# Kernel tuning notes

Measured on AMD Instinct MI355X. Metric: run time of the kernel, lower is better.

## Reference

```python
import jax, jax.numpy as jnp
import numpy as np

B, T, D, H, L, V = 2, 1024, 1024, 16, 6, 32000
HD = D // H  # head_size = n_emb // n_heads
EPS = 1e-5   # torch LayerNorm default


def setup_inputs() -> dict:
    key = jax.random.key(0)
    ks = jax.random.split(key, 19)
    s = 0.02
    n = lambda k, shape: jax.random.normal(k, shape, dtype=jnp.float32) * s
    return {
        "idx": jax.random.randint(ks[0], (B, T), 0, V),
        "targets": jax.random.randint(ks[1], (B, T), 0, V),
        "tok_emb": n(ks[2], (V, D)),
        "pos_emb": n(ks[3], (V, D)),  # only first T rows used, as in the source
        "Wq": n(ks[4], (L, H, D, HD)),
        "Wk": n(ks[5], (L, H, D, HD)),
        "Wv": n(ks[6], (L, H, D, HD)),
        "Wo": n(ks[7], (L, D, D)),
        "bo": n(ks[8], (L, D)),
        "W1": n(ks[9], (L, D, 4 * D)),
        "b1": n(ks[10], (L, 4 * D)),
        "W2": n(ks[11], (L, 4 * D, D)),
        "b2": n(ks[12], (L, D)),
        "ln_g": jnp.ones((D,), jnp.float32),
        "ln_b": jnp.zeros((D,), jnp.float32),
        "Wf": n(ks[13], (D, V)),
        "bf": n(ks[14], (V,)),
    }


def _layer_norm(x, g, b):
    mu = jnp.mean(x, axis=-1, keepdims=True)
    var = jnp.mean(jnp.square(x - mu), axis=-1, keepdims=True)
    return (x - mu) * jax.lax.rsqrt(var + EPS) * g + b


def _forward(idx, targets, tok_emb, pos_emb, Wq, Wk, Wv, Wo, bo,
             W1, b1, W2, b2, ln_g, ln_b, Wf, bf):
    x = tok_emb[idx] + pos_emb[:T]  # [B,T,D]
    tril = jnp.tril(jnp.ones((T, T), dtype=bool))
    scale = jnp.asarray(D, x.dtype) ** -0.5  # NOTE: source scales by C=N_EMBED, not head_size

    def block(x, p):
        wq, wk, wv, wo, bo_, w1, b1_, w2, b2_ = p
        q = jnp.einsum('btd,hde->bhte', x, wq)
        k = jnp.einsum('btd,hde->bhte', x, wk)
        v = jnp.einsum('btd,hde->bhte', x, wv)
        scores = jnp.einsum('bhte,bhse->bhts', q, k) * scale
        scores = jnp.where(tril, scores, -jnp.inf)
        att = jax.nn.softmax(scores, axis=-1)
        o = jnp.einsum('bhts,bhse->bhte', att, v)
        o = o.transpose(0, 2, 1, 3).reshape(B, T, D)  # concat heads
        x = x + o @ wo + bo_                           # attn residual (no LN in source)
        h = jax.nn.relu(x @ w1 + b1_)
        x = x + h @ w2 + b2_                           # ffn residual
        return x, None

    x, _ = jax.lax.scan(block, x, (Wq, Wk, Wv, Wo, bo, W1, b1, W2, b2))
    x = _layer_norm(x, ln_g, ln_b)
    logits = x @ Wf + bf  # [B,T,V]
    logp = jax.nn.log_softmax(logits, axis=-1)
    nll = -jnp.take_along_axis(logp, targets[..., None], axis=-1)
    loss = jnp.mean(nll)
    return logits, loss


def reference(idx, targets, tok_emb, pos_emb, Wq, Wk, Wv, Wo, bo,
              W1, b1, W2, b2, ln_g, ln_b, Wf, bf):
    return _forward(idx, targets, tok_emb, pos_emb, Wq, Wk, Wv, Wo, bo,
                    W1, b1, W2, b2, ln_g, ln_b, Wf, bf)
```

## Files before the change

### kernel.cpp

```cpp
#include <hip/hip_runtime.h>
#include <hip/hip_bf16.h>

typedef unsigned short u16;
typedef unsigned int u32;
typedef float f32x4 __attribute__((ext_vector_type(4)));
typedef __bf16 bf16x8 __attribute__((ext_vector_type(8)));

#define NB 2
#define NT 1024
#define ND 1024
#define NH 16
#define HDIM 64
#define NL 6
#define NV 32000
#define ND4 4096
#define BT (NB * NT)
#define L2E 1.44269504f
#define NSLOT 500

__device__ __forceinline__ u16 f2b(float f) {
  u32 u = __builtin_bit_cast(u32, f);
  u32 r = (u + 0x7FFFu + ((u >> 16) & 1u)) >> 16;
  return (u16)r;
}

__device__ __forceinline__ void gl_lds16(const void* g, void* lds) {
  __builtin_amdgcn_global_load_lds((const __attribute__((address_space(1))) u32*)g,
                                   (__attribute__((address_space(3))) u32*)lds, 16, 0, 0);
}

__device__ __forceinline__ float rmax16(float v) {
  v = fmaxf(v, __shfl_xor(v, 1, 64));
  v = fmaxf(v, __shfl_xor(v, 2, 64));
  v = fmaxf(v, __shfl_xor(v, 4, 64));
  v = fmaxf(v, __shfl_xor(v, 8, 64));
  return v;
}
__device__ __forceinline__ float rsum16(float v) {
  v += __shfl_xor(v, 1, 64);
  v += __shfl_xor(v, 2, 64);
  v += __shfl_xor(v, 4, 64);
  v += __shfl_xor(v, 8, 64);
  return v;
}

__device__ __forceinline__ void tr512(const float* in, int in_rs, u16* out, int out_rs,
                                      int k0, int n0, float (*t)[65]) {
  int tid = threadIdx.x;
#pragma unroll
  for (int i = 0; i < 8; ++i) {
    int e = tid + 512 * i;
    int r = e >> 6, c = e & 63;
    t[r][c] = in[(size_t)(k0 + r) * in_rs + n0 + c];
  }
  __syncthreads();
#pragma unroll
  for (int i = 0; i < 8; ++i) {
    int e = tid + 512 * i;
    int r = e >> 6, c = e & 63;
    out[(size_t)(n0 + r) * out_rs + k0 + c] = f2b(t[c][r]);
  }
}

__device__ __forceinline__ void trans512_blk(
    int i, int l, const float* Wq, const float* Wk, const float* Wv,
    const float* Wo, const float* W1, const float* W2,
    u16* wqkvT, u16* woT, u16* w1T, u16* w2T, float (*t)[65]) {
  if (i < 768) {
    int x = i & 15, z = i >> 4;
    int s = z >> 4, h = z & 15;
    const float* in = (s == 0 ? Wq : s == 1 ? Wk : Wv) + ((size_t)(l * NH + h)) * ND * HDIM;
    u16* o = wqkvT + ((size_t)(s * ND + h * HDIM)) * ND;
    tr512(in, HDIM, o, ND, x * 64, 0, t);
  } else if (i < 1024) {
    int j = i - 768, x = j & 15, y = j >> 4;
    tr512(Wo + (size_t)l * ND * ND, ND, woT, ND, y * 64, x * 64, t);
  } else if (i < 2048) {
    int j = i - 1024, x = j & 63, y = j >> 6;
    tr512(W1 + (size_t)l * ND * ND4, ND4, w1T, ND, y * 64, x * 64, t);
  } else {
    int j = i - 2048, x = j & 15, y = j >> 4;
    tr512(W2 + (size_t)l * ND4 * ND, ND, w2T, ND4, y * 64, x * 64, t);
  }
}

__global__ void __launch_bounds__(512) k_pre(const int* __restrict__ idx,
                                             const float* __restrict__ tok,
                                             const float* __restrict__ pos,
                                             float* __restrict__ xf, u16* __restrict__ xb,
                                             const float* __restrict__ Wq,
                                             const float* __restrict__ Wk,
                                             const float* __restrict__ Wv,
                                             const float* __restrict__ Wo,
                                             const float* __restrict__ W1,
                                             const float* __restrict__ W2,
                                             u16* __restrict__ wT0) {
  __shared__ float t[64][65];
  int bid = blockIdx.x;
  if (bid < 1024) {
    int tid = threadIdx.x;
    int row = bid * 2 + (tid >> 8);
    int tt = row & (NT - 1);
    int tk = idx[row];
    int c = (tid & 255) * 4;
    float4 a = *(const float4*)(tok + (size_t)tk * ND + c);
    float4 p = *(const float4*)(pos + (size_t)tt * ND + c);
    float4 s = make_float4(a.x + p.x, a.y + p.y, a.z + p.z, a.w + p.w);
    *(float4*)(xf + (size_t)row * ND + c) = s;
    u16* o = xb + (size_t)row * ND + c;
    *(u32*)(o + 0) = (u32)f2b(s.x) | ((u32)f2b(s.y) << 16);
    *(u32*)(o + 2) = (u32)f2b(s.z) | ((u32)f2b(s.w) << 16);
    return;
  }
  trans512_blk(bid - 1024, 0, Wq, Wk, Wv, Wo, W1, W2,
               wT0, wT0 + (size_t)3 * ND * ND, wT0 + (size_t)4 * ND * ND,
               wT0 + (size_t)8 * ND * ND, t);
}

template <int EPI>
__global__ void __launch_bounds__(512, 2)
k_gemm8(const u16* __restrict__ A, const u16* __restrict__ Bt,
        const float* __restrict__ bias, float* __restrict__ outf,
        u16* __restrict__ outb, int K, int N, int nMt, float* __restrict__ pl) {
  __shared__ u16 lds[2][2][2][128 * 64];
  int tid = threadIdx.x;
  int w = tid >> 6, l = tid & 63;
  int l4 = l >> 4, lm = l & 15;
  int wm = w >> 2, wn = w & 3;

  int nwg = gridDim.x, bid = blockIdx.x;
  int q8 = nwg >> 3, r8 = nwg & 7;
  int xcd = bid & 7, loc = bid >> 3;
  int swz = (xcd < r8 ? xcd * (q8 + 1) : r8 * (q8 + 1) + (xcd - r8) * q8) + loc;
  int m0 = (swz % nMt) * 256;
  int n0 = (swz / nMt) * 256;

  f32x4 acc[8][4];
  f32x4 z = {0.f, 0.f, 0.f, 0.f};
#pragma unroll
  for (int m = 0; m < 8; ++m)
#pragma unroll
    for (int n = 0; n < 4; ++n) acc[m][n] = z;

  int srow = (w << 3) + (l >> 3);
  int scol = (((l & 7) ^ ((l >> 3) & 7)) << 3);
  int sdst = w * 512 + l * 8;

  auto stage_half = [&](int b, int mat, int h, int kt) {
    int k0 = kt << 6;
    const u16* base = (mat == 0 ? A + (size_t)(m0 + (h << 7)) * K
                                : Bt + (size_t)(n0 + (h << 7)) * K);
#pragma unroll
    for (int i = 0; i < 2; ++i)
      gl_lds16(base + (size_t)(i * 64 + srow) * K + k0 + scol,
               &lds[b][mat][h][i * 4096 + sdst]);
  };

  int c0 = (l4 ^ (lm & 7)) * 8;
  int c1 = c0 ^ 32;
  int brow0 = (wn & 1) * 64;

  const u16* A0h = &lds[0][0][wm][0];
  const u16* B0h = &lds[0][1][wn >> 1][0];
  const u16* A1h = &lds[1][0][wm][0];
  const u16* B1h = &lds[1][1][wn >> 1][0];

  bf16x8 Ar[4][2], Bx[2][2], By[2][2];

  auto dsA = [&](const u16* Ah, int mf0) {
#pragma unroll
    for (int mf = 0; mf < 4; ++mf) {
      Ar[mf][0] = *(const bf16x8*)&Ah[((mf0 + mf) * 16 + lm) * 64 + c0];
      Ar[mf][1] = *(const bf16x8*)&Ah[((mf0 + mf) * 16 + lm) * 64 + c1];
    }
  };
  auto dsB = [&](const u16* Bh, bf16x8 (&B)[2][2], int nf0) {
#pragma unroll
    for (int nf = 0; nf < 2; ++nf) {
      B[nf][0] = *(const bf16x8*)&Bh[(brow0 + (nf0 + nf) * 16 + lm) * 64 + c0];
      B[nf][1] = *(const bf16x8*)&Bh[(brow0 + (nf0 + nf) * 16 + lm) * 64 + c1];
    }
  };
  auto mm = [&](int am, bf16x8 (&B)[2][2], int an) {
    __builtin_amdgcn_s_setprio(1);
#pragma unroll
    for (int mf = 0; mf < 4; ++mf)
#pragma unroll
      for (int nf = 0; nf < 2; ++nf) {
        acc[am + mf][an + nf] =
            __builtin_amdgcn_mfma_f32_16x16x32_bf16(Ar[mf][0], B[nf][0], acc[am + mf][an + nf], 0, 0, 0);
        acc[am + mf][an + nf] =
            __builtin_amdgcn_mfma_f32_16x16x32_bf16(Ar[mf][1], B[nf][1], acc[am + mf][an + nf], 0, 0, 0);
      }
    __builtin_amdgcn_s_setprio(0);
  };
  auto openbar = [&]() {
    __builtin_amdgcn_sched_barrier(0);
    __builtin_amdgcn_s_barrier();
    __builtin_amdgcn_sched_barrier(0);
  };
  auto midbar = [&]() {
    __builtin_amdgcn_sched_barrier(0);
    __builtin_amdgcn_s_barrier();
    asm volatile("s_waitcnt lgkmcnt(0)" ::: "memory");
    __builtin_amdgcn_sched_barrier(0);
  };

  int nk = K >> 6;
  stage_half(0, 0, 0, 0); stage_half(0, 0, 1, 0);
  stage_half(0, 1, 0, 0); stage_half(0, 1, 1, 0);
  stage_half(1, 0, 0, 1);

  for (int u = 0; u < nk; u += 2) {
    bool s2 = (u + 2 < nk), s3 = (u + 3 < nk);
    asm volatile("s_waitcnt vmcnt(2)" ::: "memory");
    openbar();
    dsA(A0h, 0); dsB(B0h, Bx, 0);
    stage_half(1, 0, 1, u + 1);
    midbar();
    mm(0, Bx, 0);
    openbar();
    dsB(B0h, By, 2);
    stage_half(1, 1, 0, u + 1);
    midbar();
    mm(0, By, 2);
    openbar();
    dsA(A0h, 4);
    stage_half(1, 1, 1, u + 1);
    midbar();
    mm(4, By, 2);
    openbar();
    if (s2) stage_half(0, 0, 0, u + 2);
    midbar();
    mm(4, Bx, 0);
    if (s2) asm volatile("s_waitcnt vmcnt(2)" ::: "memory");
    else    asm volatile("s_waitcnt vmcnt(0)" ::: "memory");
    openbar();
    dsA(A1h, 0); dsB(B1h, Bx, 0);
    if (s2) stage_half(0, 0, 1, u + 2);
    midbar();
    mm(0, Bx, 0);
    openbar();
    dsB(B1h, By, 2);
    if (s2) stage_half(0, 1, 0, u + 2);
    midbar();
    mm(0, By, 2);
    openbar();
    dsA(A1h, 4);
    if (s2) stage_half(0, 1, 1, u + 2);
    midbar();
    mm(4, By, 2);
    openbar();
    if (s3) stage_half(1, 0, 0, u + 3);
    midbar();
    mm(4, Bx, 0);
  }

  if constexpr (EPI == 4) {
    int slot = (n0 >> 6) + wn;
#pragma unroll
    for (int mf = 0; mf < 8; ++mf)
#pragma unroll
      for (int j = 0; j < 4; ++j) {
        int row = m0 + wm * 128 + mf * 16 + l4 * 4 + j;
        float sm = 0.f;
#pragma unroll
        for (int nf = 0; nf < 4; ++nf) {
          int col = n0 + wn * 64 + nf * 16 + lm;
          float v = acc[mf][nf][j] + bias[col];
          __builtin_nontemporal_store(v, &outf[(size_t)row * N + col]);
          sm += exp2f(v * L2E);
        }
        sm = rsum16(sm);
        if (lm == 0) pl[(size_t)row * NSLOT + slot] = sm;
      }
  } else {
#pragma unroll
    for (int mf = 0; mf < 8; ++mf)
#pragma unroll
      for (int nf = 0; nf < 4; ++nf)
#pragma unroll
        for (int j = 0; j < 4; ++j) {
          int row = m0 + wm * 128 + mf * 16 + l4 * 4 + j;
          int col = n0 + wn * 64 + nf * 16 + lm;
          float v = acc[mf][nf][j];
          if constexpr (EPI == 0) outb[(size_t)row * N + col] = f2b(v);
          else __builtin_nontemporal_store(v + bias[col], &outf[(size_t)row * N + col]);
        }
  }
}

template <int EPI, int BN>
__global__ void __launch_bounds__(256, BN == 64 ? 3 : 2)
k_gemm4(const u16* __restrict__ A, const u16* __restrict__ Bt,
        const float* __restrict__ bias, float* __restrict__ outf,
        u16* __restrict__ outb, int K, int N, int nMt) {
  constexpr int NFW = BN / 32;
  constexpr int NH2 = NFW / 2;
  __shared__ u16 As[2][128 * 64];
  __shared__ u16 Bs[2][BN * 64];
  int tid = threadIdx.x;
  int w = tid >> 6, l = tid & 63;
  int l4 = l >> 4, lm = l & 15;
  int wr = w >> 1, wc = w & 1;

  int nwg = gridDim.x, bid = blockIdx.x;
  int q8 = nwg >> 3, r8 = nwg & 7;
  int xcd = bid & 7, loc = bid >> 3;
  int swz = (xcd < r8 ? xcd * (q8 + 1) : r8 * (q8 + 1) + (xcd - r8) * q8) + loc;
  int m0 = (swz % nMt) * 128;
  int n0 = (swz / nMt) * BN;

  f32x4 acc[4][NFW];
  f32x4 z = {0.f, 0.f, 0.f, 0.f};
#pragma unroll
  for (int m = 0; m < 4; ++m)
#pragma unroll
    for (int n = 0; n < NFW; ++n) acc[m][n] = z;

  int srow = (w << 3) + (l >> 3);
  int scol = (((l & 7) ^ ((l >> 3) & 7)) << 3);
  int sdst = w * 512 + l * 8;

  const u16* Arow = A + (size_t)m0 * K;
  const u16* Brow = Bt + (size_t)n0 * K;

  auto stage = [&](int b, int kt) {
    int k0 = kt << 6;
#pragma unroll
    for (int i = 0; i < 4; ++i)
      gl_lds16(Arow + (size_t)(i * 32 + srow) * K + k0 + scol, &As[b][i * 2048 + sdst]);
#pragma unroll
    for (int i = 0; i < BN / 32; ++i)
      gl_lds16(Brow + (size_t)(i * 32 + srow) * K + k0 + scol, &Bs[b][i * 2048 + sdst]);
  };

  int c0 = (l4 ^ (lm & 7)) * 8;
  int c1 = c0 ^ 32;

  int nk = K >> 6;
  stage(0, 0);
  for (int t = 0; t < nk; ++t) {
    int b = t & 1;
    asm volatile("s_waitcnt vmcnt(0)" ::: "memory");
    __builtin_amdgcn_sched_barrier(0);
    __builtin_amdgcn_s_barrier();
    __builtin_amdgcn_sched_barrier(0);
    if (t + 1 < nk) stage(b ^ 1, t + 1);
    __builtin_amdgcn_sched_barrier(0);

    bf16x8 af[4][2], bfr[NH2][2];
#pragma unroll
    for (int mf = 0; mf < 4; ++mf) {
      af[mf][0] = *(const bf16x8*)&As[b][(mf * 16 + lm) * 64 + c0 + (wr * 64 * 64)];
      af[mf][1] = *(const bf16x8*)&As[b][(mf * 16 + lm) * 64 + c1 + (wr * 64 * 64)];
    }
#pragma unroll
    for (int nf = 0; nf < NH2; ++nf) {
      int brow = wc * (BN / 2) + nf * 16 + lm;
      bfr[nf][0] = *(const bf16x8*)&Bs[b][brow * 64 + c0];
      bfr[nf][1] = *(const bf16x8*)&Bs[b][brow * 64 + c1];
    }
    __builtin_amdgcn_s_setprio(1);
#pragma unroll
    for (int mf = 0; mf < 4; ++mf)
#pragma unroll
      for (int nf = 0; nf < NH2; ++nf) {
        acc[mf][nf] = __builtin_amdgcn_mfma_f32_16x16x32_bf16(af[mf][0], bfr[nf][0], acc[mf][nf], 0, 0, 0);
        acc[mf][nf] = __builtin_amdgcn_mfma_f32_16x16x32_bf16(af[mf][1], bfr[nf][1], acc[mf][nf], 0, 0, 0);
      }
    __builtin_amdgcn_s_setprio(0);

#pragma unroll
    for (int nf = 0; nf < NH2; ++nf) {
      int brow = wc * (BN / 2) + (nf + NH2) * 16 + lm;
      bfr[nf][0] = *(const bf16x8*)&Bs[b][brow * 64 + c0];
      bfr[nf][1] = *(const bf16x8*)&Bs[b][brow * 64 + c1];
    }
    __builtin_amdgcn_s_setprio(1);
#pragma unroll
    for (int mf = 0; mf < 4; ++mf)
#pragma unroll
      for (int nf = 0; nf < NH2; ++nf) {
        acc[mf][nf + NH2] = __builtin_amdgcn_mfma_f32_16x16x32_bf16(af[mf][0], bfr[nf][0], acc[mf][nf + NH2], 0, 0, 0);
        acc[mf][nf + NH2] = __builtin_amdgcn_mfma_f32_16x16x32_bf16(af[mf][1], bfr[nf][1], acc[mf][nf + NH2], 0, 0, 0);
      }
    __builtin_amdgcn_s_setprio(0);
  }

#pragma unroll
  for (int mf = 0; mf < 4; ++mf)
#pragma unroll
    for (int nf = 0; nf < NFW; ++nf)
#pragma unroll
      for (int j = 0; j < 4; ++j) {
        int row = m0 + wr * 64 + mf * 16 + l4 * 4 + j;
        int col = n0 + wc * (BN / 2) + nf * 16 + lm;
        float v = acc[mf][nf][j];
        if constexpr (EPI == 0) {
          outb[(size_t)row * N + col] = f2b(v);
        } else if constexpr (EPI == 2) {
          v += bias[col];
          outb[(size_t)row * N + col] = f2b(fmaxf(v, 0.f));
        } else {
          v += bias[col];
          size_t o = (size_t)row * N + col;
          float nx = outf[o] + v;
          outf[o] = nx;
          outb[o] = f2b(nx);
        }
      }
}

__global__ void __launch_bounds__(512) k_attn_mega(
    const u16* __restrict__ qkv, u16* __restrict__ ob,
    const float* __restrict__ Wq, const float* __restrict__ Wk,
    const float* __restrict__ Wv, const float* __restrict__ Wo,
    const float* __restrict__ W1, const float* __restrict__ W2,
    const float* __restrict__ Wf, u16* __restrict__ wTnext,
    u16* __restrict__ wfT, int lNext) {
  __shared__ char smem[70656];
  int bid = blockIdx.x;
  if (bid >= 256) {
    auto t = reinterpret_cast<float(*)[65]>(smem);
    int i = bid - 256;
    if (lNext < NL) {
      trans512_blk(i, lNext, Wq, Wk, Wv, Wo, W1, W2,
                   wTnext, wTnext + (size_t)3 * ND * ND, wTnext + (size_t)4 * ND * ND,
                   wTnext + (size_t)8 * ND * ND, t);
    } else {
      int x = i % 500, y = i / 500;
      tr512(Wf, NV, wfT, ND, y * 64, x * 64, t);
    }
    return;
  }
  u16* Ks = (u16*)smem;
  u16* Vt = Ks + 128 * 72;
  u16* Pw = Vt + 64 * 136;
  int qb = bid & 7, h = (bid >> 3) & 15, b = bid >> 7;
  int tid = threadIdx.x;
  int w = tid >> 6, l = tid & 63;
  int l4 = l >> 4, lm = l & 15;

  const u16* base = qkv + (size_t)b * NT * 3072 + h * HDIM;

  bf16x8 qf[2];
#pragma unroll
  for (int kk = 0; kk < 2; ++kk) {
    int tq = qb * 128 + w * 16 + lm;
    qf[kk] = *(const bf16x8*)(base + (size_t)tq * 3072 + kk * 32 + l4 * 8);
  }

  int r0 = tid >> 3, e0 = (tid & 7) << 3;

  auto loadT = [&](int kb, bf16x8& k0, bf16x8& k1, bf16x8& v0, bf16x8& v1) {
    const u16* s0 = base + (size_t)(kb * 128 + r0) * 3072;
    const u16* s1 = s0 + (size_t)64 * 3072;
    k0 = *(const bf16x8*)(s0 + 1024 + e0);
    v0 = *(const bf16x8*)(s0 + 2048 + e0);
    k1 = *(const bf16x8*)(s1 + 1024 + e0);
    v1 = *(const bf16x8*)(s1 + 2048 + e0);
  };

  f32x4 z = {0.f, 0.f, 0.f, 0.f};
  f32x4 oacc[4];
  float mrow[4], lrow[4];
#pragma unroll
  for (int n = 0; n < 4; ++n) oacc[n] = z;
#pragma unroll
  for (int j = 0; j < 4; ++j) { mrow[j] = -1e30f; lrow[j] = 0.f; }

  bf16x8 ck0, ck1, cv0, cv1;
  loadT(0, ck0, ck1, cv0, cv1);
  bf16x8 nk0 = ck0, nk1 = ck1, nv0 = cv0, nv1 = cv1;

  for (int kb = 0; kb <= qb; ++kb) {
    __syncthreads();
    {
      *(bf16x8*)&Ks[r0 * 72 + e0] = ck0;
      *(bf16x8*)&Ks[(r0 + 64) * 72 + e0] = ck1;
      union { bf16x8 v; u16 u[8]; } a, c;
      a.v = cv0; c.v = cv1;
#pragma unroll
      for (int j = 0; j < 8; ++j) {
        Vt[(e0 + j) * 136 + r0] = a.u[j];
        Vt[(e0 + j) * 136 + r0 + 64] = c.u[j];
      }
    }
    if (kb < qb) loadT(kb + 1, nk0, nk1, nv0, nv1);
    __syncthreads();

    f32x4 s[8];
#pragma unroll
    for (int n = 0; n < 8; ++n) s[n] = z;
#pragma unroll
    for (int kk = 0; kk < 2; ++kk)
#pragma unroll
      for (int n = 0; n < 8; ++n) {
        bf16x8 kf = *(const bf16x8*)&Ks[(n * 16 + lm) * 72 + kk * 32 + l4 * 8];
        s[n] = __builtin_amdgcn_mfma_f32_16x16x32_bf16(qf[kk], kf, s[n], 0, 0, 0);
      }

    bool diag = (kb == qb);
#pragma unroll
    for (int j = 0; j < 4; ++j) {
      int rloc = w * 16 + l4 * 4 + j;
      float pv[8];
      float rm = -1e30f;
#pragma unroll
      for (int n = 0; n < 8; ++n) {
        float vv = s[n][j] * 0.03125f;
        if (diag && (n * 16 + lm > rloc)) vv = -1e30f;
        pv[n] = vv;
        rm = fmaxf(rm, vv);
      }
      rm = rmax16(rm);
      float nm = fmaxf(mrow[j], rm);
      float corr = exp2f((mrow[j] - nm) * L2E);
      mrow[j] = nm;
      float rs = 0.f;
#pragma unroll
      for (int n = 0; n < 8; ++n) {
        float p = exp2f((pv[n] - nm) * L2E);
        pv[n] = p;
        rs += p;
      }
      rs = rsum16(rs);
      lrow[j] = lrow[j] * corr + rs;
#pragma unroll
      for (int n = 0; n < 4; ++n) oacc[n][j] *= corr;
      int prow = l4 * 4 + j;
#pragma unroll
      for (int n = 0; n < 8; ++n) Pw[(w * 16 + prow) * 136 + n * 16 + lm] = f2b(pv[n]);
    }
    asm volatile("s_waitcnt lgkmcnt(0)" ::: "memory");
    __builtin_amdgcn_sched_barrier(0);

#pragma unroll
    for (int kk = 0; kk < 4; ++kk) {
      bf16x8 pa = *(const bf16x8*)&Pw[(w * 16 + lm) * 136 + kk * 32 + l4 * 8];
#pragma unroll
      for (int n = 0; n < 4; ++n) {
        bf16x8 vf = *(const bf16x8*)&Vt[(n * 16 + lm) * 136 + kk * 32 + l4 * 8];
        oacc[n] = __builtin_amdgcn_mfma_f32_16x16x32_bf16(pa, vf, oacc[n], 0, 0, 0);
      }
    }

    ck0 = nk0; ck1 = nk1; cv0 = nv0; cv1 = nv1;
  }

#pragma unroll
  for (int n = 0; n < 4; ++n)
#pragma unroll
    for (int j = 0; j < 4; ++j) {
      int tq = qb * 128 + w * 16 + l4 * 4 + j;
      int col = h * HDIM + n * 16 + lm;
      float v = oacc[n][j] / lrow[j];
      ob[(size_t)(b * NT + tq) * ND + col] = f2b(v);
    }
}

__global__ void k_ln(const float* __restrict__ xf, const float* __restrict__ g,
                     const float* __restrict__ bta, u16* __restrict__ xb) {
  __shared__ float red[4];
  int row = blockIdx.x, tid = threadIdx.x;
  int w = tid >> 6;
  int c = tid * 4;
  float4 x = *(const float4*)(xf + (size_t)row * ND + c);
  float s = x.x + x.y + x.z + x.w;
#pragma unroll
  for (int off = 1; off < 64; off <<= 1) s += __shfl_xor(s, off, 64);
  if ((tid & 63) == 0) red[w] = s;
  __syncthreads();
  float mu = (red[0] + red[1] + red[2] + red[3]) * (1.0f / ND);
  float d0 = x.x - mu, d1 = x.y - mu, d2 = x.z - mu, d3 = x.w - mu;
  float v = d0 * d0 + d1 * d1 + d2 * d2 + d3 * d3;
  __syncthreads();
#pragma unroll
  for (int off = 1; off < 64; off <<= 1) v += __shfl_xor(v, off, 64);
  if ((tid & 63) == 0) red[w] = v;
  __syncthreads();
  float var = (red[0] + red[1] + red[2] + red[3]) * (1.0f / ND);
  float rs = rsqrtf(var + 1e-5f);
  float4 gg = *(const float4*)(g + c);
  float4 bb = *(const float4*)(bta + c);
  u16* o = xb + (size_t)row * ND + c;
  o[0] = f2b(d0 * rs * gg.x + bb.x);
  o[1] = f2b(d1 * rs * gg.y + bb.y);
  o[2] = f2b(d2 * rs * gg.z + bb.z);
  o[3] = f2b(d3 * rs * gg.w + bb.w);
}

__global__ void k_loss_row2(const float* __restrict__ pl, const float* __restrict__ logits,
                            const int* __restrict__ tgt, float* __restrict__ lossbuf) {
  int row = blockIdx.x, l = threadIdx.x;
  const float* pr = pl + (size_t)row * NSLOT;
  float s = 0.f;
  for (int i = l; i < NSLOT; i += 64) s += pr[i];
#pragma unroll
  for (int off = 1; off < 64; off <<= 1) s += __shfl_xor(s, off, 64);
  if (l == 0) lossbuf[row] = logf(s) - logits[(size_t)row * NV + tgt[row]];
}

__global__ void k_loss_final(const float* __restrict__ lossbuf, float* __restrict__ out) {
  __shared__ float red[4];
  int tid = threadIdx.x;
  float s = 0.f;
  for (int i = tid; i < BT; i += 256) s += lossbuf[i];
#pragma unroll
  for (int off = 1; off < 64; off <<= 1) s += __shfl_xor(s, off, 64);
  if ((tid & 63) == 0) red[tid >> 6] = s;
  __syncthreads();
  if (tid == 0) out[0] = (red[0] + red[1] + red[2] + red[3]) * (1.0f / BT);
}

extern "C" void kernel_launch(void* const* d_in, const int* in_sizes, int n_in,
                              void* d_out, int out_size, void* d_ws, size_t ws_size,
                              hipStream_t stream) {
  const int* idx = (const int*)d_in[0];
  const int* tgt = (const int*)d_in[1];
  const float* tok = (const float*)d_in[2];
  const float* pos = (const float*)d_in[3];
  const float* Wq = (const float*)d_in[4];
  const float* Wk = (const float*)d_in[5];
  const float* Wv = (const float*)d_in[6];
  const float* Wo = (const float*)d_in[7];
  const float* bo = (const float*)d_in[8];
  const float* W1 = (const float*)d_in[9];
  const float* b1 = (const float*)d_in[10];
  const float* W2 = (const float*)d_in[11];
  const float* b2 = (const float*)d_in[12];
  const float* lng = (const float*)d_in[13];
  const float* lnb = (const float*)d_in[14];
  const float* Wf = (const float*)d_in[15];
  const float* bfp = (const float*)d_in[16];
  float* logits = (float*)d_out;
  float* lossp = logits + (size_t)BT * NV;

  char* ws = (char*)d_ws;
  u16* wT0 = (u16*)ws;
  u16* wT1 = wT0 + (size_t)12 * ND * ND;
  u16* wfT = wT1 + (size_t)12 * ND * ND;
  size_t off = (size_t)24 * ND * ND * 2 + (size_t)NV * ND * 2;
  float* xf = (float*)(ws + off); off += (size_t)BT * ND * 4;
  u16* xb = (u16*)(ws + off);     off += (size_t)BT * ND * 2;
  u16* qkv = (u16*)(ws + off);    off += (size_t)BT * 3 * ND * 2;
  u16* obuf = (u16*)(ws + off);   off += (size_t)BT * ND * 2;
  u16* hb = (u16*)(ws + off);     off += (size_t)BT * ND4 * 2;
  float* pl = (float*)(ws + off); off += (size_t)BT * NSLOT * 4;
  float* lossbuf = (float*)(ws + off);

  k_pre<<<4096, 512, 0, stream>>>(idx, tok, pos, xf, xb, Wq, Wk, Wv, Wo, W1, W2, wT0);
  for (int l = 0; l < NL; ++l) {
    u16* wTl = (l & 1) ? wT1 : wT0;
    u16* wTn = (l & 1) ? wT0 : wT1;
    u16* wqkvT = wTl;
    u16* woT = wTl + (size_t)3 * ND * ND;
    u16* w1T = wTl + (size_t)4 * ND * ND;
    u16* w2T = wTl + (size_t)8 * ND * ND;
    k_gemm4<0, 128><<<384, 256, 0, stream>>>(xb, wqkvT, nullptr, nullptr, qkv, ND, 3 * ND, 16);
    int extra = (l + 1 < NL) ? 3072 : 8000;
    k_attn_mega<<<256 + extra, 512, 0, stream>>>(qkv, obuf, Wq, Wk, Wv, Wo, W1, W2, Wf,
                                                 wTn, wfT, l + 1);
    k_gemm4<3, 64><<<256, 256, 0, stream>>>(obuf, woT, bo + (size_t)l * ND, xf, xb, ND, ND, 16);
    k_gemm4<2, 128><<<512, 256, 0, stream>>>(xb, w1T, b1 + (size_t)l * ND4, nullptr, hb, ND, ND4, 16);
    k_gemm4<3, 64><<<256, 256, 0, stream>>>(hb, w2T, b2 + (size_t)l * ND, xf, xb, ND4, ND, 16);
  }
  k_ln<<<BT, 256, 0, stream>>>(xf, lng, lnb, xb);
  k_gemm8<4><<<1000, 512, 0, stream>>>(xb, wfT, bfp, logits, nullptr, ND, NV, 8, pl);
  k_loss_row2<<<BT, 64, 0, stream>>>(pl, logits, tgt, lossbuf);
  k_loss_final<<<1, 256, 0, stream>>>(lossbuf, lossp);
}
```

Before: 1.206 ms.

## Pair causal attention query blocks per workgroup and shrink N=1024 GEMM tiles

The attention kernel now gives each workgroup two query blocks (pr and 7-pr). Every workgroup then does the same amount of causal work, and the attention grid halves from 256 to 128 blocks. The GEMM kernel gains a BM template parameter, so the Wo and W2 projections (N=1024) run with 64x64 tiles on 512 workgroups instead of 128x64 on 256, aiming for better CU fill. The costs are fewer, longer attention workgroups with serialized passes and more redundant A/B loads from the smaller GEMM tiles.

Result: faster. 1.127 ms (-6.5%).

```diff
diff --git a/kernel.cpp b/kernel.cpp
--- a/kernel.cpp
+++ b/kernel.cpp
@@ -290,14 +290,15 @@
   }
 }
 
-template <int EPI, int BN>
-__global__ void __launch_bounds__(256, BN == 64 ? 3 : 2)
+template <int EPI, int BM, int BN>
+__global__ void __launch_bounds__(256, BM == 64 ? 4 : 2)
 k_gemm4(const u16* __restrict__ A, const u16* __restrict__ Bt,
         const float* __restrict__ bias, float* __restrict__ outf,
         u16* __restrict__ outb, int K, int N, int nMt) {
   constexpr int NFW = BN / 32;
   constexpr int NH2 = NFW / 2;
-  __shared__ u16 As[2][128 * 64];
+  constexpr int AF = BM / 32;
+  __shared__ u16 As[2][BM * 64];
   __shared__ u16 Bs[2][BN * 64];
   int tid = threadIdx.x;
   int w = tid >> 6, l = tid & 63;
@@ -308,13 +309,13 @@
   int q8 = nwg >> 3, r8 = nwg & 7;
   int xcd = bid & 7, loc = bid >> 3;
   int swz = (xcd < r8 ? xcd * (q8 + 1) : r8 * (q8 + 1) + (xcd - r8) * q8) + loc;
-  int m0 = (swz % nMt) * 128;
+  int m0 = (swz % nMt) * BM;
   int n0 = (swz / nMt) * BN;
 
-  f32x4 acc[4][NFW];
+  f32x4 acc[AF][NFW];
   f32x4 z = {0.f, 0.f, 0.f, 0.f};
 #pragma unroll
-  for (int m = 0; m < 4; ++m)
+  for (int m = 0; m < AF; ++m)
 #pragma unroll
     for (int n = 0; n < NFW; ++n) acc[m][n] = z;
 
@@ -328,7 +329,7 @@
   auto stage = [&](int b, int kt) {
     int k0 = kt << 6;
 #pragma unroll
-    for (int i = 0; i < 4; ++i)
+    for (int i = 0; i < BM / 32; ++i)
       gl_lds16(Arow + (size_t)(i * 32 + srow) * K + k0 + scol, &As[b][i * 2048 + sdst]);
 #pragma unroll
     for (int i = 0; i < BN / 32; ++i)
@@ -349,11 +350,11 @@
     if (t + 1 < nk) stage(b ^ 1, t + 1);
     __builtin_amdgcn_sched_barrier(0);
 
-    bf16x8 af[4][2], bfr[NH2][2];
-#pragma unroll
-    for (int mf = 0; mf < 4; ++mf) {
-      af[mf][0] = *(const bf16x8*)&As[b][(mf * 16 + lm) * 64 + c0 + (wr * 64 * 64)];
-      af[mf][1] = *(const bf16x8*)&As[b][(mf * 16 + lm) * 64 + c1 + (wr * 64 * 64)];
+    bf16x8 af[AF][2], bfr[NH2][2];
+#pragma unroll
+    for (int mf = 0; mf < AF; ++mf) {
+      af[mf][0] = *(const bf16x8*)&As[b][(mf * 16 + lm) * 64 + c0 + wr * (BM / 2) * 64];
+      af[mf][1] = *(const bf16x8*)&As[b][(mf * 16 + lm) * 64 + c1 + wr * (BM / 2) * 64];
     }
 #pragma unroll
     for (int nf = 0; nf < NH2; ++nf) {
@@ -363,7 +364,7 @@
     }
     __builtin_amdgcn_s_setprio(1);
 #pragma unroll
-    for (int mf = 0; mf < 4; ++mf)
+    for (int mf = 0; mf < AF; ++mf)
 #pragma unroll
       for (int nf = 0; nf < NH2; ++nf) {
         acc[mf][nf] = __builtin_amdgcn_mfma_f32_16x16x32_bf16(af[mf][0], bfr[nf][0], acc[mf][nf], 0, 0, 0);
@@ -379,7 +380,7 @@
     }
     __builtin_amdgcn_s_setprio(1);
 #pragma unroll
-    for (int mf = 0; mf < 4; ++mf)
+    for (int mf = 0; mf < AF; ++mf)
 #pragma unroll
       for (int nf = 0; nf < NH2; ++nf) {
         acc[mf][nf + NH2] = __builtin_amdgcn_mfma_f32_16x16x32_bf16(af[mf][0], bfr[nf][0], acc[mf][nf + NH2], 0, 0, 0);
@@ -389,12 +390,12 @@
   }
 
 #pragma unroll
-  for (int mf = 0; mf < 4; ++mf)
+  for (int mf = 0; mf < AF; ++mf)
 #pragma unroll
     for (int nf = 0; nf < NFW; ++nf)
 #pragma unroll
       for (int j = 0; j < 4; ++j) {
-        int row = m0 + wr * 64 + mf * 16 + l4 * 4 + j;
+        int row = m0 + wr * (BM / 2) + mf * 16 + l4 * 4 + j;
         int col = n0 + wc * (BN / 2) + nf * 16 + lm;
         float v = acc[mf][nf][j];
         if constexpr (EPI == 0) {
@@ -421,9 +422,9 @@
     u16* __restrict__ wfT, int lNext) {
   __shared__ char smem[70656];
   int bid = blockIdx.x;
-  if (bid >= 256) {
+  if (bid >= 128) {
     auto t = reinterpret_cast<float(*)[65]>(smem);
-    int i = bid - 256;
+    int i = bid - 128;
     if (lNext < NL) {
       trans512_blk(i, lNext, Wq, Wk, Wv, Wo, W1, W2,
                    wTnext, wTnext + (size_t)3 * ND * ND, wTnext + (size_t)4 * ND * ND,
@@ -437,20 +438,12 @@
   u16* Ks = (u16*)smem;
   u16* Vt = Ks + 128 * 72;
   u16* Pw = Vt + 64 * 136;
-  int qb = bid & 7, h = (bid >> 3) & 15, b = bid >> 7;
+  int pr = bid & 3, h = (bid >> 2) & 15, b = bid >> 6;
   int tid = threadIdx.x;
   int w = tid >> 6, l = tid & 63;
   int l4 = l >> 4, lm = l & 15;
 
   const u16* base = qkv + (size_t)b * NT * 3072 + h * HDIM;
-
-  bf16x8 qf[2];
-#pragma unroll
-  for (int kk = 0; kk < 2; ++kk) {
-    int tq = qb * 128 + w * 16 + lm;
-    qf[kk] = *(const bf16x8*)(base + (size_t)tq * 3072 + kk * 32 + l4 * 8);
-  }
-
   int r0 = tid >> 3, e0 = (tid & 7) << 3;
 
   auto loadT = [&](int kb, bf16x8& k0, bf16x8& k1, bf16x8& v0, bf16x8& v1) {
@@ -463,101 +456,113 @@
   };
 
   f32x4 z = {0.f, 0.f, 0.f, 0.f};
-  f32x4 oacc[4];
-  float mrow[4], lrow[4];
-#pragma unroll
-  for (int n = 0; n < 4; ++n) oacc[n] = z;
-#pragma unroll
-  for (int j = 0; j < 4; ++j) { mrow[j] = -1e30f; lrow[j] = 0.f; }
-
-  bf16x8 ck0, ck1, cv0, cv1;
-  loadT(0, ck0, ck1, cv0, cv1);
-  bf16x8 nk0 = ck0, nk1 = ck1, nv0 = cv0, nv1 = cv1;
-
-  for (int kb = 0; kb <= qb; ++kb) {
-    __syncthreads();
-    {
-      *(bf16x8*)&Ks[r0 * 72 + e0] = ck0;
-      *(bf16x8*)&Ks[(r0 + 64) * 72 + e0] = ck1;
-      union { bf16x8 v; u16 u[8]; } a, c;
-      a.v = cv0; c.v = cv1;
-#pragma unroll
-      for (int j = 0; j < 8; ++j) {
-        Vt[(e0 + j) * 136 + r0] = a.u[j];
-        Vt[(e0 + j) * 136 + r0 + 64] = c.u[j];
-      }
-    }
-    if (kb < qb) loadT(kb + 1, nk0, nk1, nv0, nv1);
-    __syncthreads();
-
-    f32x4 s[8];
-#pragma unroll
-    for (int n = 0; n < 8; ++n) s[n] = z;
-#pragma unroll
-    for (int kk = 0; kk < 2; ++kk)
-#pragma unroll
-      for (int n = 0; n < 8; ++n) {
-        bf16x8 kf = *(const bf16x8*)&Ks[(n * 16 + lm) * 72 + kk * 32 + l4 * 8];
-        s[n] = __builtin_amdgcn_mfma_f32_16x16x32_bf16(qf[kk], kf, s[n], 0, 0, 0);
-      }
-
-    bool diag = (kb == qb);
-#pragma unroll
-    for (int j = 0; j < 4; ++j) {
-      int rloc = w * 16 + l4 * 4 + j;
-      float pv[8];
-      float rm = -1e30f;
-#pragma unroll
-      for (int n = 0; n < 8; ++n) {
-        float vv = s[n][j] * 0.03125f;
-        if (diag && (n * 16 + lm > rloc)) vv = -1e30f;
-        pv[n] = vv;
-        rm = fmaxf(rm, vv);
-      }
-      rm = rmax16(rm);
-      float nm = fmaxf(mrow[j], rm);
-      float corr = exp2f((mrow[j] - nm) * L2E);
-      mrow[j] = nm;
-      float rs = 0.f;
-#pragma unroll
-      for (int n = 0; n < 8; ++n) {
-        float p = exp2f((pv[n] - nm) * L2E);
-        pv[n] = p;
-        rs += p;
-      }
-      rs = rsum16(rs);
-      lrow[j] = lrow[j] * corr + rs;
-#pragma unroll
-      for (int n = 0; n < 4; ++n) oacc[n][j] *= corr;
-      int prow = l4 * 4 + j;
-#pragma unroll
-      for (int n = 0; n < 8; ++n) Pw[(w * 16 + prow) * 136 + n * 16 + lm] = f2b(pv[n]);
-    }
-    asm volatile("s_waitcnt lgkmcnt(0)" ::: "memory");
-    __builtin_amdgcn_sched_barrier(0);
-
-#pragma unroll
-    for (int kk = 0; kk < 4; ++kk) {
-      bf16x8 pa = *(const bf16x8*)&Pw[(w * 16 + lm) * 136 + kk * 32 + l4 * 8];
-#pragma unroll
-      for (int n = 0; n < 4; ++n) {
-        bf16x8 vf = *(const bf16x8*)&Vt[(n * 16 + lm) * 136 + kk * 32 + l4 * 8];
-        oacc[n] = __builtin_amdgcn_mfma_f32_16x16x32_bf16(pa, vf, oacc[n], 0, 0, 0);
-      }
-    }
-
-    ck0 = nk0; ck1 = nk1; cv0 = nv0; cv1 = nv1;
-  }
-
-#pragma unroll
-  for (int n = 0; n < 4; ++n)
-#pragma unroll
-    for (int j = 0; j < 4; ++j) {
-      int tq = qb * 128 + w * 16 + l4 * 4 + j;
-      int col = h * HDIM + n * 16 + lm;
-      float v = oacc[n][j] / lrow[j];
-      ob[(size_t)(b * NT + tq) * ND + col] = f2b(v);
-    }
+
+  for (int pass = 0; pass < 2; ++pass) {
+    int qb = pass ? (7 - pr) : pr;
+
+    bf16x8 qf[2];
+#pragma unroll
+    for (int kk = 0; kk < 2; ++kk) {
+      int tq = qb * 128 + w * 16 + lm;
+      qf[kk] = *(const bf16x8*)(base + (size_t)tq * 3072 + kk * 32 + l4 * 8);
+    }
+
+    f32x4 oacc[4];
+    float mrow[4], lrow[4];
+#pragma unroll
+    for (int n = 0; n < 4; ++n) oacc[n] = z;
+#pragma unroll
+    for (int j = 0; j < 4; ++j) { mrow[j] = -1e30f; lrow[j] = 0.f; }
+
+    bf16x8 ck0, ck1, cv0, cv1;
+    loadT(0, ck0, ck1, cv0, cv1);
+    bf16x8 nk0 = ck0, nk1 = ck1, nv0 = cv0, nv1 = cv1;
+
+    for (int kb = 0; kb <= qb; ++kb) {
+      __syncthreads();
+      {
+        *(bf16x8*)&Ks[r0 * 72 + e0] = ck0;
+        *(bf16x8*)&Ks[(r0 + 64) * 72 + e0] = ck1;
+        union { bf16x8 v; u16 u[8]; } a, c;
+        a.v = cv0; c.v = cv1;
+#pragma unroll
+        for (int j = 0; j < 8; ++j) {
+          Vt[(e0 + j) * 136 + r0] = a.u[j];
+          Vt[(e0 + j) * 136 + r0 + 64] = c.u[j];
+        }
+      }
+      if (kb < qb) loadT(kb + 1, nk0, nk1, nv0, nv1);
+      __syncthreads();
+
+      f32x4 s[8];
+#pragma unroll
+      for (int n = 0; n < 8; ++n) s[n] = z;
+#pragma unroll
+      for (int kk = 0; kk < 2; ++kk)
+#pragma unroll
+        for (int n = 0; n < 8; ++n) {
+          bf16x8 kf = *(const bf16x8*)&Ks[(n * 16 + lm) * 72 + kk * 32 + l4 * 8];
+          s[n] = __builtin_amdgcn_mfma_f32_16x16x32_bf16(qf[kk], kf, s[n], 0, 0, 0);
+        }
+
+      bool diag = (kb == qb);
+#pragma unroll
+      for (int j = 0; j < 4; ++j) {
+        int rloc = w * 16 + l4 * 4 + j;
+        float pv[8];
+        float rm = -1e30f;
+#pragma unroll
+        for (int n = 0; n < 8; ++n) {
+          float vv = s[n][j] * 0.03125f;
+          if (diag && (n * 16 + lm > rloc)) vv = -1e30f;
+          pv[n] = vv;
+          rm = fmaxf(rm, vv);
+        }
+        rm = rmax16(rm);
+        float nm = fmaxf(mrow[j], rm);
+        float corr = exp2f((mrow[j] - nm) * L2E);
+        mrow[j] = nm;
+        float rs = 0.f;
+#pragma unroll
+        for (int n = 0; n < 8; ++n) {
+          float p = exp2f((pv[n] - nm) * L2E);
+          pv[n] = p;
+          rs += p;
+        }
+        rs = rsum16(rs);
+        lrow[j] = lrow[j] * corr + rs;
+#pragma unroll
+        for (int n = 0; n < 4; ++n) oacc[n][j] *= corr;
+        int prow = l4 * 4 + j;
+#pragma unroll
+        for (int n = 0; n < 8; ++n) Pw[(w * 16 + prow) * 136 + n * 16 + lm] = f2b(pv[n]);
+      }
+      asm volatile("s_waitcnt lgkmcnt(0)" ::: "memory");
+      __builtin_amdgcn_sched_barrier(0);
+
+#pragma unroll
+      for (int kk = 0; kk < 4; ++kk) {
+        bf16x8 pa = *(const bf16x8*)&Pw[(w * 16 + lm) * 136 + kk * 32 + l4 * 8];
+#pragma unroll
+        for (int n = 0; n < 4; ++n) {
+          bf16x8 vf = *(const bf16x8*)&Vt[(n * 16 + lm) * 136 + kk * 32 + l4 * 8];
+          oacc[n] = __builtin_amdgcn_mfma_f32_16x16x32_bf16(pa, vf, oacc[n], 0, 0, 0);
+        }
+      }
+
+      ck0 = nk0; ck1 = nk1; cv0 = nv0; cv1 = nv1;
+    }
+
+#pragma unroll
+    for (int n = 0; n < 4; ++n)
+#pragma unroll
+      for (int j = 0; j < 4; ++j) {
+        int tq = qb * 128 + w * 16 + l4 * 4 + j;
+        int col = h * HDIM + n * 16 + lm;
+        float v = oacc[n][j] / lrow[j];
+        ob[(size_t)(b * NT + tq) * ND + col] = f2b(v);
+      }
+  }
 }
 
 __global__ void k_ln(const float* __restrict__ xf, const float* __restrict__ g,
@@ -658,13 +663,13 @@
     u16* woT = wTl + (size_t)3 * ND * ND;
     u16* w1T = wTl + (size_t)4 * ND * ND;
     u16* w2T = wTl + (size_t)8 * ND * ND;
-    k_gemm4<0, 128><<<384, 256, 0, stream>>>(xb, wqkvT, nullptr, nullptr, qkv, ND, 3 * ND, 16);
+    k_gemm4<0, 128, 128><<<384, 256, 0, stream>>>(xb, wqkvT, nullptr, nullptr, qkv, ND, 3 * ND, 16);
     int extra = (l + 1 < NL) ? 3072 : 8000;
-    k_attn_mega<<<256 + extra, 512, 0, stream>>>(qkv, obuf, Wq, Wk, Wv, Wo, W1, W2, Wf,
+    k_attn_mega<<<128 + extra, 512, 0, stream>>>(qkv, obuf, Wq, Wk, Wv, Wo, W1, W2, Wf,
                                                  wTn, wfT, l + 1);
-    k_gemm4<3, 64><<<256, 256, 0, stream>>>(obuf, woT, bo + (size_t)l * ND, xf, xb, ND, ND, 16);
-    k_gemm4<2, 128><<<512, 256, 0, stream>>>(xb, w1T, b1 + (size_t)l * ND4, nullptr, hb, ND, ND4, 16);
-    k_gemm4<3, 64><<<256, 256, 0, stream>>>(hb, w2T, b2 + (size_t)l * ND, xf, xb, ND4, ND, 16);
+    k_gemm4<3, 64, 64><<<512, 256, 0, stream>>>(obuf, woT, bo + (size_t)l * ND, xf, xb, ND, ND, 32);
+    k_gemm4<2, 128, 128><<<512, 256, 0, stream>>>(xb, w1T, b1 + (size_t)l * ND4, nullptr, hb, ND, ND4, 16);
+    k_gemm4<3, 64, 64><<<512, 256, 0, stream>>>(hb, w2T, b2 + (size_t)l * ND, xf, xb, ND4, ND, 32);
   }
   k_ln<<<BT, 256, 0, stream>>>(xf, lng, lnb, xb);
   k_gemm8<4><<<1000, 512, 0, stream>>>(xb, wfT, bfp, logits, nullptr, ND, NV, 8, pl);
```
